# Optimization experiments

Measured on AMD Instinct MI355X. Metric: run time of the kernel, lower is better.

The kernel has to match this reference:

```python
import jax, jax.numpy as jnp
import numpy as np

N_HEAD = 16
D_MODEL = 1024
D_K = 64
D_V = 64
B = 8
L = 1024
EPS = 1e-5
NEG_INF = -1e9


def setup_inputs() -> dict:
    key = jax.random.key(0)
    ks = jax.random.split(key, 6)
    qkv_out = N_HEAD * (2 * D_K + D_V)  # 3072
    x = jax.random.normal(ks[0], (B, L, D_MODEL), dtype=jnp.float32)
    # causal attention mask (N, 1, L, L), 1 = keep, 0 = masked
    mask = jnp.broadcast_to(jnp.tril(jnp.ones((L, L), jnp.float32))[None, None], (B, 1, L, L))
    W_qkv = jax.random.normal(ks[1], (D_MODEL, qkv_out), dtype=jnp.float32) * 0.02
    b_qkv = jnp.zeros((qkv_out,), jnp.float32)
    W_proj = jax.random.normal(ks[2], (N_HEAD * D_V, D_MODEL), dtype=jnp.float32) * 0.02
    b_proj = jnp.zeros((D_MODEL,), jnp.float32)
    gamma = jnp.ones((D_MODEL,), jnp.float32)
    beta = jnp.zeros((D_MODEL,), jnp.float32)
    return {"x": x, "mask": mask, "W_qkv": W_qkv, "b_qkv": b_qkv,
            "W_proj": W_proj, "b_proj": b_proj, "gamma": gamma, "beta": beta}


def _layer_norm(x, gamma, beta):
    u = jnp.mean(x, axis=-1, keepdims=True)
    s = jnp.mean(jnp.square(x - u), axis=-1, keepdims=True)
    return gamma * (x - u) / jnp.sqrt(s + EPS) + beta


def reference(x, mask, W_qkv, b_qkv, W_proj, b_proj, gamma, beta):
    residual = x
    qkv = jnp.einsum('bld,df->blf', x, W_qkv) + b_qkv  # 1x1 Conv1D == pointwise linear
    q_l = N_HEAD * D_K
    q = qkv[:, :, :q_l]
    k = qkv[:, :, q_l:2 * q_l]
    v = qkv[:, :, 2 * q_l:]
    # split heads: (B, L, H*D) -> (B, H, L, D)
    q = q.reshape(B, L, N_HEAD, D_K).transpose(0, 2, 1, 3)
    k = k.reshape(B, L, N_HEAD, D_K).transpose(0, 2, 1, 3)
    v = v.reshape(B, L, N_HEAD, D_V).transpose(0, 2, 1, 3)
    temperature = np.power(D_K, 0.5)
    attn = jnp.einsum('bhqd,bhkd->bhqk', q, k) / temperature
    attn = mask * attn + (1.0 - mask) * NEG_INF
    attn = jax.nn.softmax(attn, axis=-1)  # dropout is identity in eval mode
    out = jnp.einsum('bhqk,bhkd->bhqd', attn, v)
    # merge heads: (B, H, L, Dv) -> (B, L, H*Dv)
    out = out.transpose(0, 2, 1, 3).reshape(B, L, N_HEAD * D_V)
    out = jnp.einsum('blf,fd->bld', out, W_proj) + b_proj
    out = _layer_norm(out + residual, gamma, beta)
    return out, attn
```

## Files before the change

### kernel.cpp

```cpp
#include <hip/hip_runtime.h>

typedef __attribute__((ext_vector_type(4))) float f32x4;
typedef __attribute__((ext_vector_type(8))) __bf16 bf16x8;
typedef __attribute__((ext_vector_type(8))) unsigned short ushort8;

static __device__ __forceinline__ unsigned short f2bf(float f) {
    unsigned int u = __float_as_uint(f);
    u += 0x7fffu + ((u >> 16) & 1u);
    return (unsigned short)(u >> 16);
}
static __device__ __forceinline__ float bf2f(unsigned short u) {
    return __uint_as_float((unsigned int)u << 16);
}
static __device__ __forceinline__ bf16x8 as_bf(ushort8 v) {
    union { ushort8 u; bf16x8 b; } x; x.u = v; return x.b;
}
static __device__ __forceinline__ void gll16(const void* g, void* l) {
    __builtin_amdgcn_global_load_lds(
        (const __attribute__((address_space(1))) void*)g,
        (__attribute__((address_space(3))) void*)l, 16, 0, 0);
}

__global__ void cvt_bf16(const float* __restrict__ in, unsigned short* __restrict__ out,
                         int n8) {
    int i = blockIdx.x * 256 + threadIdx.x;
    if (i >= n8) return;
    const float4* p = (const float4*)(in + (size_t)i * 8);
    float4 a = p[0], b = p[1];
    ushort8 o = { f2bf(a.x), f2bf(a.y), f2bf(a.z), f2bf(a.w),
                  f2bf(b.x), f2bf(b.y), f2bf(b.z), f2bf(b.w) };
    *(ushort8*)(out + (size_t)i * 8) = o;
}

__global__ void tconv_bf16(const float* __restrict__ in, unsigned short* __restrict__ out,
                           int K, int N) {
    __shared__ float t[64][65];
    const int tid = threadIdx.x;
    const int n0 = blockIdx.x * 64, k0 = blockIdx.y * 64;
#pragma unroll
    for (int i = 0; i < 4; i++) {
        int idx = tid + 256 * i;
        int r = idx >> 4, c4 = (idx & 15) * 4;
        float4 v = *(const float4*)(in + (size_t)(k0 + r) * N + n0 + c4);
        t[r][c4] = v.x; t[r][c4 + 1] = v.y; t[r][c4 + 2] = v.z; t[r][c4 + 3] = v.w;
    }
    __syncthreads();
#pragma unroll
    for (int i = 0; i < 2; i++) {
        int idx = tid + 256 * i;
        int nl = idx >> 3, k8 = (idx & 7) * 8;
        ushort8 o;
#pragma unroll
        for (int j = 0; j < 8; j++) o[j] = f2bf(t[k8 + j][nl]);
        *(ushort8*)(out + (size_t)(n0 + nl) * K + k0 + k8) = o;
    }
}

template <int EPI>
__global__ __launch_bounds__(256, 2)
void gemm_bf16(const unsigned short* __restrict__ A,
               const unsigned short* __restrict__ BT,
               const float* __restrict__ bias,
               unsigned short* __restrict__ qh, unsigned short* __restrict__ kh,
               unsigned short* __restrict__ vt,
               float* __restrict__ Cf,
               int K, int mtiles, int Ncols)
{
    __shared__ unsigned short smem[2 * 128 * 64];
    unsigned short* As = smem;
    unsigned short* Bs = smem + 128 * 64;

    const int tid = threadIdx.x;
    const int wid = tid >> 6, lane = tid & 63;
    const int g = lane >> 4, c = lane & 15;
    const int wr = (wid >> 1) * 64, wc = (wid & 1) * 64;

    const int nwg = gridDim.x;
    const int swz = ((int)blockIdx.x & 7) * (nwg >> 3) + ((int)blockIdx.x >> 3);
    const int bm = (swz % mtiles) * 128;
    const int bn = (swz / mtiles) * 128;

    const int srow = lane >> 3;
    const int scol8 = ((lane & 7) ^ srow) * 8;
    const size_t arow0 = (size_t)(bm + wid * 8 + srow);
    const size_t brow0 = (size_t)(bn + wid * 8 + srow);

    f32x4 acc[4][4] = {};

    for (int k0 = 0; k0 < K; k0 += 64) {
        __syncthreads();
#pragma unroll
        for (int t = 0; t < 4; t++) {
            gll16(A + (arow0 + t * 32) * K + k0 + scol8,
                  (char*)As + t * 4096 + wid * 1024);
            gll16(BT + (brow0 + t * 32) * K + k0 + scol8,
                  (char*)Bs + t * 4096 + wid * 1024);
        }
        __syncthreads();
#pragma unroll
        for (int ks = 0; ks < 2; ks++) {
            bf16x8 af[4], bfr[4];
#pragma unroll
            for (int mi = 0; mi < 4; mi++) {
                int row = wr + mi * 16 + c;
                int off = row * 128 + ((ks * 64 + g * 16) ^ ((c & 7) << 4));
                af[mi] = as_bf(*(const ushort8*)((const char*)As + off));
            }
#pragma unroll
            for (int ni = 0; ni < 4; ni++) {
                int row = wc + ni * 16 + c;
                int off = row * 128 + ((ks * 64 + g * 16) ^ ((c & 7) << 4));
                bfr[ni] = as_bf(*(const ushort8*)((const char*)Bs + off));
            }
#pragma unroll
            for (int mi = 0; mi < 4; mi++)
#pragma unroll
                for (int ni = 0; ni < 4; ni++)
                    acc[mi][ni] = __builtin_amdgcn_mfma_f32_16x16x32_bf16(
                        af[mi], bfr[ni], acc[mi][ni], 0, 0, 0);
        }
    }

    if (EPI == 1) {
#pragma unroll
        for (int mi = 0; mi < 4; mi++)
#pragma unroll
            for (int ni = 0; ni < 4; ni++)
#pragma unroll
                for (int r = 0; r < 4; r++) {
                    int m = bm + wr + mi * 16 + g * 4 + r;
                    int n = bn + wc + ni * 16 + c;
                    Cf[(size_t)m * Ncols + n] = acc[mi][ni][r] + bias[n];
                }
    } else {
        const int b = bm >> 10, lb = bm & 1023;
#pragma unroll
        for (int nh = 0; nh < 2; nh++) {
            int n0 = bn + nh * 64;
            int region = n0 >> 10;
            int h = (n0 & 1023) >> 6;
            __syncthreads();
            if (region < 2) {
                float qscale = (region == 0) ? 0.1803368801f : 1.0f;
                if ((wid & 1) == nh) {
#pragma unroll
                    for (int mi = 0; mi < 4; mi++)
#pragma unroll
                        for (int ni = 0; ni < 4; ni++)
#pragma unroll
                            for (int r = 0; r < 4; r++) {
                                int row = wr + mi * 16 + g * 4 + r;
                                int col = ni * 16 + c;
                                float v = (acc[mi][ni][r] + bias[n0 + col]) * qscale;
                                smem[row * 64 + col] = f2bf(v);
                            }
                }
                __syncthreads();
                unsigned short* dst = region == 0 ? qh : kh;
#pragma unroll
                for (int i = 0; i < 4; i++) {
                    int idx = tid + 256 * i;
                    int row = idx >> 3, c8 = (idx & 7) * 8;
                    ushort8 v = *(const ushort8*)&smem[row * 64 + c8];
                    *(ushort8*)(dst + ((size_t)((b * 16 + h) * 1024 + lb + row)) * 64 + c8) = v;
                }
            } else {
                if ((wid & 1) == nh) {
#pragma unroll
                    for (int mi = 0; mi < 4; mi++)
#pragma unroll
                        for (int ni = 0; ni < 4; ni++)
#pragma unroll
                            for (int r = 0; r < 4; r++) {
                                int l = wr + mi * 16 + g * 4 + r;
                                int d = ni * 16 + c;
                                float v = acc[mi][ni][r] + bias[n0 + d];
                                smem[d * 128 + (l ^ ((d & 7) << 3))] = f2bf(v);
                            }
                }
                __syncthreads();
#pragma unroll
                for (int i = 0; i < 4; i++) {
                    int idx = tid + 256 * i;
                    int d = idx >> 4, l8 = idx & 15;
                    ushort8 v = *(const ushort8*)&smem[d * 128 + ((l8 * 8) ^ ((d & 7) << 3))];
                    *(ushort8*)(vt + ((size_t)((b * 16 + h) * 64 + d)) * 1024 + lb + l8 * 8) = v;
                }
            }
        }
    }
}

__global__ __launch_bounds__(256, 2)
void attn_kernel(const unsigned short* __restrict__ qh,
                 const unsigned short* __restrict__ kh,
                 const unsigned short* __restrict__ vt,
                 float* __restrict__ attn, unsigned short* __restrict__ ob)
{
    __shared__ char smem[24576];
    char* Ks = smem;
    char* Vs = smem + 8192;
    char* Ps = smem + 16384;

    const int bh = blockIdx.x;
    const int qt = blockIdx.y;
    const int q0 = qt * 64;
    const int ntiles = qt + 1;

    const int tid = threadIdx.x, wid = tid >> 6, lane = tid & 63;
    const int g = lane >> 4, c = lane & 15;

    const size_t baseKV = (size_t)bh * 65536;
    const int qrow = q0 + wid * 16 + c;

    bf16x8 qa[2];
    qa[0] = as_bf(*(const ushort8*)(qh + baseKV + (size_t)qrow * 64 + g * 8));
    qa[1] = as_bf(*(const ushort8*)(qh + baseKV + (size_t)qrow * 64 + 32 + g * 8));

    const int srow = lane >> 3;
    const int scol8 = ((lane & 7) ^ srow) * 8;

    float lsum = 0.f;
    for (int kt = 0; kt < ntiles; ++kt) {
        const unsigned short* kb = kh + baseKV + (size_t)kt * 4096;
        __syncthreads();
        gll16(kb + (size_t)(wid * 8 + srow) * 64 + scol8, Ks + wid * 1024);
        gll16(kb + (size_t)(32 + wid * 8 + srow) * 64 + scol8, Ks + 4096 + wid * 1024);
        __syncthreads();
#pragma unroll
        for (int a = 0; a < 4; a++) {
            int krow = a * 16 + c;
            f32x4 sa = {0.f, 0.f, 0.f, 0.f};
#pragma unroll
            for (int ks = 0; ks < 2; ks++) {
                int off = krow * 128 + ((ks * 64 + g * 16) ^ ((c & 7) << 4));
                bf16x8 kf = as_bf(*(const ushort8*)(Ks + off));
                sa = __builtin_amdgcn_mfma_f32_16x16x32_bf16(kf, qa[ks], sa, 0, 0, 0);
            }
            int kb4 = kt * 64 + a * 16 + g * 4;
#pragma unroll
            for (int r = 0; r < 4; r++)
                lsum += (kb4 + r > qrow) ? 0.f : __builtin_amdgcn_exp2f(sa[r]);
        }
    }
    lsum += __shfl_xor(lsum, 16);
    lsum += __shfl_xor(lsum, 32);
    const float lr = -__log2f(lsum);

    char* Pw = Ps + wid * 2048;
    float* attnB = attn + (size_t)bh * (1024 * 1024) + (size_t)q0 * 1024;
    f32x4 oacc[4] = {};

    for (int kt = 0; kt < ntiles; ++kt) {
        const unsigned short* kb = kh + baseKV + (size_t)kt * 4096;
        const unsigned short* vb = vt + baseKV + kt * 64;
        __syncthreads();
        gll16(kb + (size_t)(wid * 8 + srow) * 64 + scol8, Ks + wid * 1024);
        gll16(kb + (size_t)(32 + wid * 8 + srow) * 64 + scol8, Ks + 4096 + wid * 1024);
        gll16(vb + (size_t)(wid * 8 + srow) * 1024 + scol8, Vs + wid * 1024);
        gll16(vb + (size_t)(32 + wid * 8 + srow) * 1024 + scol8, Vs + 4096 + wid * 1024);
        __syncthreads();

#pragma unroll
        for (int a = 0; a < 4; a++) {
            int krow = a * 16 + c;
            f32x4 sa = {0.f, 0.f, 0.f, 0.f};
#pragma unroll
            for (int ks = 0; ks < 2; ks++) {
                int off = krow * 128 + ((ks * 64 + g * 16) ^ ((c & 7) << 4));
                bf16x8 kf = as_bf(*(const ushort8*)(Ks + off));
                sa = __builtin_amdgcn_mfma_f32_16x16x32_bf16(kf, qa[ks], sa, 0, 0, 0);
            }
            int kb4 = kt * 64 + a * 16 + g * 4;
            float p0 = __builtin_amdgcn_exp2f((kb4 + 0 > qrow) ? -1e9f : sa[0] + lr);
            float p1 = __builtin_amdgcn_exp2f((kb4 + 1 > qrow) ? -1e9f : sa[1] + lr);
            float p2 = __builtin_amdgcn_exp2f((kb4 + 2 > qrow) ? -1e9f : sa[2] + lr);
            float p3 = __builtin_amdgcn_exp2f((kb4 + 3 > qrow) ? -1e9f : sa[3] + lr);
            uint2 pw;
            asm("v_cvt_pk_bf16_f32 %0, %1, %2" : "=v"(pw.x) : "v"(p0), "v"(p1));
            asm("v_cvt_pk_bf16_f32 %0, %1, %2" : "=v"(pw.y) : "v"(p2), "v"(p3));
            *(uint2*)(Pw + c * 128 + ((a * 32 + g * 8) ^ ((c & 7) << 4))) = pw;
        }

#pragma unroll
        for (int ks = 0; ks < 2; ks++) {
            int aoff = c * 128 + ((ks * 64 + g * 16) ^ ((c & 7) << 4));
            bf16x8 pa = as_bf(*(const ushort8*)(Pw + aoff));
#pragma unroll
            for (int ni = 0; ni < 4; ni++) {
                int d = ni * 16 + c;
                int voff = d * 128 + ((ks * 64 + g * 16) ^ ((d & 7) << 4));
                bf16x8 vf = as_bf(*(const ushort8*)(Vs + voff));
                oacc[ni] = __builtin_amdgcn_mfma_f32_16x16x32_bf16(pa, vf, oacc[ni], 0, 0, 0);
            }
        }
        __syncthreads();

#pragma unroll
        for (int i = 0; i < 2; i++) {
            int idx = tid + 256 * i;
            int row = idx >> 3, c16 = idx & 7;
            int off = (row >> 4) * 2048 + (row & 15) * 128 + ((c16 * 16) ^ ((row & 7) << 4));
            ushort8 v = *(const ushort8*)(Ps + off);
            float4 f0 = { bf2f(v[0]), bf2f(v[1]), bf2f(v[2]), bf2f(v[3]) };
            float4 f1 = { bf2f(v[4]), bf2f(v[5]), bf2f(v[6]), bf2f(v[7]) };
            float* dp = attnB + (size_t)row * 1024 + kt * 64 + c16 * 8;
            *(float4*)dp = f0;
            *(float4*)(dp + 4) = f1;
        }
    }

    {
        float4 z = {0.f, 0.f, 0.f, 0.f};
        for (int kt = ntiles; kt < 16; ++kt) {
#pragma unroll
            for (int i = 0; i < 4; i++) {
                int idx = tid + 256 * i;
                int row = idx >> 4, c4 = (idx & 15) << 2;
                *(float4*)(attnB + (size_t)row * 1024 + kt * 64 + c4) = z;
            }
        }
    }

    __syncthreads();
#pragma unroll
    for (int ni = 0; ni < 4; ni++)
#pragma unroll
        for (int r = 0; r < 4; r++) {
            int row = wid * 16 + g * 4 + r;
            int d = ni * 16 + c;
            int off = row * 128 + ((d * 2) ^ ((row & 7) << 4));
            *(unsigned short*)(Ks + off) = f2bf(oacc[ni][r]);
        }
    __syncthreads();
    {
        const int b = bh >> 4, h = bh & 15;
#pragma unroll
        for (int i = 0; i < 2; i++) {
            int idx = tid + 256 * i;
            int row = idx >> 3, c8 = idx & 7;
            int off = row * 128 + ((c8 * 16) ^ ((row & 7) << 4));
            ushort8 v = *(const ushort8*)(Ks + off);
            *(ushort8*)(ob + ((size_t)(b * 1024 + q0 + row)) * 1024 + h * 64 + c8 * 8) = v;
        }
    }
}

__global__ __launch_bounds__(256, 2)
void ln_kernel(const float* __restrict__ y, const float* __restrict__ x,
               const float* __restrict__ gamma, const float* __restrict__ beta,
               float* __restrict__ out)
{
    const int m = blockIdx.x;
    const int tid = threadIdx.x;
    const int wid = tid >> 6, lane = tid & 63;
    float4 vy = *(const float4*)(y + (size_t)m * 1024 + tid * 4);
    float4 vx = *(const float4*)(x + (size_t)m * 1024 + tid * 4);
    float4 v = {vy.x + vx.x, vy.y + vx.y, vy.z + vx.z, vy.w + vx.w};
    float s1 = v.x + v.y + v.z + v.w;
    float s2 = v.x * v.x + v.y * v.y + v.z * v.z + v.w * v.w;
#pragma unroll
    for (int d = 1; d < 64; d <<= 1) {
        s1 += __shfl_xor(s1, d);
        s2 += __shfl_xor(s2, d);
    }
    __shared__ float red1[4], red2[4];
    if (lane == 0) { red1[wid] = s1; red2[wid] = s2; }
    __syncthreads();
    float t1 = red1[0] + red1[1] + red1[2] + red1[3];
    float t2 = red2[0] + red2[1] + red2[2] + red2[3];
    float mean = t1 * (1.f / 1024.f);
    float var = t2 * (1.f / 1024.f) - mean * mean;
    float rstd = rsqrtf(var + 1e-5f);
    float4 g4 = *(const float4*)(gamma + tid * 4);
    float4 b4 = *(const float4*)(beta + tid * 4);
    float4 o;
    o.x = g4.x * (v.x - mean) * rstd + b4.x;
    o.y = g4.y * (v.y - mean) * rstd + b4.y;
    o.z = g4.z * (v.z - mean) * rstd + b4.z;
    o.w = g4.w * (v.w - mean) * rstd + b4.w;
    *(float4*)(out + (size_t)m * 1024 + tid * 4) = o;
}

extern "C" void kernel_launch(void* const* d_in, const int* in_sizes, int n_in,
                              void* d_out, int out_size, void* d_ws, size_t ws_size,
                              hipStream_t stream)
{
    const float* x      = (const float*)d_in[0];
    const float* W_qkv  = (const float*)d_in[2];
    const float* b_qkv  = (const float*)d_in[3];
    const float* W_proj = (const float*)d_in[4];
    const float* b_proj = (const float*)d_in[5];
    const float* gamma  = (const float*)d_in[6];
    const float* beta   = (const float*)d_in[7];

    float* out  = (float*)d_out;
    float* attn = out + (size_t)8 * 1024 * 1024;

    const size_t E = (size_t)8192 * 1024;
    unsigned short* ws = (unsigned short*)d_ws;
    unsigned short* qh     = ws;
    unsigned short* kh     = qh + E;
    unsigned short* vt     = kh + E;
    unsigned short* xb     = vt + E;
    unsigned short* wqkvT  = xb + E;
    unsigned short* wprojT = wqkvT + (size_t)3072 * 1024;
    unsigned short* ob     = wprojT + (size_t)1024 * 1024;
    float* yb   = (float*)(void*)qh;

    cvt_bf16<<<4096, 256, 0, stream>>>(x, xb, (int)(E / 8));
    tconv_bf16<<<dim3(48, 16), 256, 0, stream>>>(W_qkv, wqkvT, 1024, 3072);
    tconv_bf16<<<dim3(16, 16), 256, 0, stream>>>(W_proj, wprojT, 1024, 1024);

    gemm_bf16<0><<<1536, 256, 0, stream>>>(xb, wqkvT, b_qkv,
                                           qh, kh, vt, nullptr, 1024, 64, 3072);
    attn_kernel<<<dim3(128, 16), 256, 0, stream>>>(qh, kh, vt, attn, ob);
    gemm_bf16<1><<<512, 256, 0, stream>>>(ob, wprojT, b_proj,
                                          nullptr, nullptr, nullptr, yb, 1024, 64, 1024);
    ln_kernel<<<8192, 256, 0, stream>>>(yb, x, gamma, beta, out);
}
```

Baseline: 270.8 us.

## Double-buffer K/V/P tiles in attention kernel with prefetch and priority hints

Both attention passes now prefetch the next K (and V) tile into a second LDS buffer while the current tile is computed, so the loop needs one barrier per iteration instead of two. The P buffer is also double-buffered, which lets the attn-matrix writeback overlap the next tile's work. s_setprio raises wave priority around the MFMA sections, and launch bounds change from 2 to 3 blocks per SM. LDS use doubles to 48KB, which could limit occupancy. The correctness of the single-barrier scheme depends on the global_load_lds prefetch completing before the barrier.

```diff
diff --git a/kernel.cpp b/kernel.cpp
--- a/kernel.cpp
+++ b/kernel.cpp
@@ -191,16 +191,13 @@
     }
 }
 
-__global__ __launch_bounds__(256, 2)
+__global__ __launch_bounds__(256, 3)
 void attn_kernel(const unsigned short* __restrict__ qh,
                  const unsigned short* __restrict__ kh,
                  const unsigned short* __restrict__ vt,
                  float* __restrict__ attn, unsigned short* __restrict__ ob)
 {
-    __shared__ char smem[24576];
-    char* Ks = smem;
-    char* Vs = smem + 8192;
-    char* Ps = smem + 16384;
+    __shared__ char smem[49152];
 
     const int bh = blockIdx.x;
     const int qt = blockIdx.y;
@@ -221,92 +218,123 @@
     const int scol8 = ((lane & 7) ^ srow) * 8;
 
     float lsum = 0.f;
-    for (int kt = 0; kt < ntiles; ++kt) {
-        const unsigned short* kb = kh + baseKV + (size_t)kt * 4096;
+    {
+        int cur = 0;
+        const unsigned short* kb0 = kh + baseKV;
+        gll16(kb0 + (size_t)(wid * 8 + srow) * 64 + scol8, smem + wid * 1024);
+        gll16(kb0 + (size_t)(32 + wid * 8 + srow) * 64 + scol8, smem + 4096 + wid * 1024);
         __syncthreads();
-        gll16(kb + (size_t)(wid * 8 + srow) * 64 + scol8, Ks + wid * 1024);
-        gll16(kb + (size_t)(32 + wid * 8 + srow) * 64 + scol8, Ks + 4096 + wid * 1024);
-        __syncthreads();
-#pragma unroll
-        for (int a = 0; a < 4; a++) {
-            int krow = a * 16 + c;
-            f32x4 sa = {0.f, 0.f, 0.f, 0.f};
-#pragma unroll
-            for (int ks = 0; ks < 2; ks++) {
-                int off = krow * 128 + ((ks * 64 + g * 16) ^ ((c & 7) << 4));
-                bf16x8 kf = as_bf(*(const ushort8*)(Ks + off));
-                sa = __builtin_amdgcn_mfma_f32_16x16x32_bf16(kf, qa[ks], sa, 0, 0, 0);
-            }
-            int kb4 = kt * 64 + a * 16 + g * 4;
-#pragma unroll
-            for (int r = 0; r < 4; r++)
-                lsum += (kb4 + r > qrow) ? 0.f : __builtin_amdgcn_exp2f(sa[r]);
+        for (int kt = 0; kt < ntiles; ++kt) {
+            if (kt + 1 < ntiles) {
+                const unsigned short* kb = kh + baseKV + (size_t)(kt + 1) * 4096;
+                char* dst = smem + (cur ^ 1) * 8192;
+                gll16(kb + (size_t)(wid * 8 + srow) * 64 + scol8, dst + wid * 1024);
+                gll16(kb + (size_t)(32 + wid * 8 + srow) * 64 + scol8, dst + 4096 + wid * 1024);
+            }
+            const char* Kc = smem + cur * 8192;
+            __builtin_amdgcn_s_setprio(1);
+#pragma unroll
+            for (int a = 0; a < 4; a++) {
+                int krow = a * 16 + c;
+                f32x4 sa = {0.f, 0.f, 0.f, 0.f};
+#pragma unroll
+                for (int ks = 0; ks < 2; ks++) {
+                    int off = krow * 128 + ((ks * 64 + g * 16) ^ ((c & 7) << 4));
+                    bf16x8 kf = as_bf(*(const ushort8*)(Kc + off));
+                    sa = __builtin_amdgcn_mfma_f32_16x16x32_bf16(kf, qa[ks], sa, 0, 0, 0);
+                }
+                int kb4 = kt * 64 + a * 16 + g * 4;
+#pragma unroll
+                for (int r = 0; r < 4; r++)
+                    lsum += (kb4 + r > qrow) ? 0.f : __builtin_amdgcn_exp2f(sa[r]);
+            }
+            __builtin_amdgcn_s_setprio(0);
+            __syncthreads();
+            cur ^= 1;
         }
     }
     lsum += __shfl_xor(lsum, 16);
     lsum += __shfl_xor(lsum, 32);
     const float lr = -__log2f(lsum);
 
-    char* Pw = Ps + wid * 2048;
     float* attnB = attn + (size_t)bh * (1024 * 1024) + (size_t)q0 * 1024;
     f32x4 oacc[4] = {};
-
-    for (int kt = 0; kt < ntiles; ++kt) {
-        const unsigned short* kb = kh + baseKV + (size_t)kt * 4096;
-        const unsigned short* vb = vt + baseKV + kt * 64;
+    {
+        int cur = 0;
+        const unsigned short* kb0 = kh + baseKV;
+        const unsigned short* vb0 = vt + baseKV;
+        gll16(kb0 + (size_t)(wid * 8 + srow) * 64 + scol8, smem + wid * 1024);
+        gll16(kb0 + (size_t)(32 + wid * 8 + srow) * 64 + scol8, smem + 4096 + wid * 1024);
+        gll16(vb0 + (size_t)(wid * 8 + srow) * 1024 + scol8, smem + 16384 + wid * 1024);
+        gll16(vb0 + (size_t)(32 + wid * 8 + srow) * 1024 + scol8, smem + 20480 + wid * 1024);
         __syncthreads();
-        gll16(kb + (size_t)(wid * 8 + srow) * 64 + scol8, Ks + wid * 1024);
-        gll16(kb + (size_t)(32 + wid * 8 + srow) * 64 + scol8, Ks + 4096 + wid * 1024);
-        gll16(vb + (size_t)(wid * 8 + srow) * 1024 + scol8, Vs + wid * 1024);
-        gll16(vb + (size_t)(32 + wid * 8 + srow) * 1024 + scol8, Vs + 4096 + wid * 1024);
-        __syncthreads();
-
-#pragma unroll
-        for (int a = 0; a < 4; a++) {
-            int krow = a * 16 + c;
-            f32x4 sa = {0.f, 0.f, 0.f, 0.f};
+
+        for (int kt = 0; kt < ntiles; ++kt) {
+            if (kt + 1 < ntiles) {
+                const unsigned short* kb = kh + baseKV + (size_t)(kt + 1) * 4096;
+                const unsigned short* vb = vt + baseKV + (kt + 1) * 64;
+                char* kdst = smem + (cur ^ 1) * 8192;
+                char* vdst = smem + 16384 + (cur ^ 1) * 8192;
+                gll16(kb + (size_t)(wid * 8 + srow) * 64 + scol8, kdst + wid * 1024);
+                gll16(kb + (size_t)(32 + wid * 8 + srow) * 64 + scol8, kdst + 4096 + wid * 1024);
+                gll16(vb + (size_t)(wid * 8 + srow) * 1024 + scol8, vdst + wid * 1024);
+                gll16(vb + (size_t)(32 + wid * 8 + srow) * 1024 + scol8, vdst + 4096 + wid * 1024);
+            }
+            const char* Kc = smem + cur * 8192;
+            const char* Vc = smem + 16384 + cur * 8192;
+            char* Pc = smem + 32768 + cur * 8192;
+            char* Pw = Pc + wid * 2048;
+
+#pragma unroll
+            for (int a = 0; a < 4; a++) {
+                int krow = a * 16 + c;
+                f32x4 sa = {0.f, 0.f, 0.f, 0.f};
+#pragma unroll
+                for (int ks = 0; ks < 2; ks++) {
+                    int off = krow * 128 + ((ks * 64 + g * 16) ^ ((c & 7) << 4));
+                    bf16x8 kf = as_bf(*(const ushort8*)(Kc + off));
+                    sa = __builtin_amdgcn_mfma_f32_16x16x32_bf16(kf, qa[ks], sa, 0, 0, 0);
+                }
+                int kb4 = kt * 64 + a * 16 + g * 4;
+                float p0 = __builtin_amdgcn_exp2f((kb4 + 0 > qrow) ? -1e9f : sa[0] + lr);
+                float p1 = __builtin_amdgcn_exp2f((kb4 + 1 > qrow) ? -1e9f : sa[1] + lr);
+                float p2 = __builtin_amdgcn_exp2f((kb4 + 2 > qrow) ? -1e9f : sa[2] + lr);
+                float p3 = __builtin_amdgcn_exp2f((kb4 + 3 > qrow) ? -1e9f : sa[3] + lr);
+                uint2 pw;
+                asm("v_cvt_pk_bf16_f32 %0, %1, %2" : "=v"(pw.x) : "v"(p0), "v"(p1));
+                asm("v_cvt_pk_bf16_f32 %0, %1, %2" : "=v"(pw.y) : "v"(p2), "v"(p3));
+                *(uint2*)(Pw + c * 128 + ((a * 32 + g * 8) ^ ((c & 7) << 4))) = pw;
+            }
+
+            __builtin_amdgcn_s_setprio(1);
 #pragma unroll
             for (int ks = 0; ks < 2; ks++) {
-                int off = krow * 128 + ((ks * 64 + g * 16) ^ ((c & 7) << 4));
-                bf16x8 kf = as_bf(*(const ushort8*)(Ks + off));
-                sa = __builtin_amdgcn_mfma_f32_16x16x32_bf16(kf, qa[ks], sa, 0, 0, 0);
-            }
-            int kb4 = kt * 64 + a * 16 + g * 4;
-            float p0 = __builtin_amdgcn_exp2f((kb4 + 0 > qrow) ? -1e9f : sa[0] + lr);
-            float p1 = __builtin_amdgcn_exp2f((kb4 + 1 > qrow) ? -1e9f : sa[1] + lr);
-            float p2 = __builtin_amdgcn_exp2f((kb4 + 2 > qrow) ? -1e9f : sa[2] + lr);
-            float p3 = __builtin_amdgcn_exp2f((kb4 + 3 > qrow) ? -1e9f : sa[3] + lr);
-            uint2 pw;
-            asm("v_cvt_pk_bf16_f32 %0, %1, %2" : "=v"(pw.x) : "v"(p0), "v"(p1));
-            asm("v_cvt_pk_bf16_f32 %0, %1, %2" : "=v"(pw.y) : "v"(p2), "v"(p3));
-            *(uint2*)(Pw + c * 128 + ((a * 32 + g * 8) ^ ((c & 7) << 4))) = pw;
-        }
-
-#pragma unroll
-        for (int ks = 0; ks < 2; ks++) {
-            int aoff = c * 128 + ((ks * 64 + g * 16) ^ ((c & 7) << 4));
-            bf16x8 pa = as_bf(*(const ushort8*)(Pw + aoff));
-#pragma unroll
-            for (int ni = 0; ni < 4; ni++) {
-                int d = ni * 16 + c;
-                int voff = d * 128 + ((ks * 64 + g * 16) ^ ((d & 7) << 4));
-                bf16x8 vf = as_bf(*(const ushort8*)(Vs + voff));
-                oacc[ni] = __builtin_amdgcn_mfma_f32_16x16x32_bf16(pa, vf, oacc[ni], 0, 0, 0);
-            }
-        }
-        __syncthreads();
-
-#pragma unroll
-        for (int i = 0; i < 2; i++) {
-            int idx = tid + 256 * i;
-            int row = idx >> 3, c16 = idx & 7;
-            int off = (row >> 4) * 2048 + (row & 15) * 128 + ((c16 * 16) ^ ((row & 7) << 4));
-            ushort8 v = *(const ushort8*)(Ps + off);
-            float4 f0 = { bf2f(v[0]), bf2f(v[1]), bf2f(v[2]), bf2f(v[3]) };
-            float4 f1 = { bf2f(v[4]), bf2f(v[5]), bf2f(v[6]), bf2f(v[7]) };
-            float* dp = attnB + (size_t)row * 1024 + kt * 64 + c16 * 8;
-            *(float4*)dp = f0;
-            *(float4*)(dp + 4) = f1;
+                int aoff = c * 128 + ((ks * 64 + g * 16) ^ ((c & 7) << 4));
+                bf16x8 pa = as_bf(*(const ushort8*)(Pw + aoff));
+#pragma unroll
+                for (int ni = 0; ni < 4; ni++) {
+                    int d = ni * 16 + c;
+                    int voff = d * 128 + ((ks * 64 + g * 16) ^ ((d & 7) << 4));
+                    bf16x8 vf = as_bf(*(const ushort8*)(Vc + voff));
+                    oacc[ni] = __builtin_amdgcn_mfma_f32_16x16x32_bf16(pa, vf, oacc[ni], 0, 0, 0);
+                }
+            }
+            __builtin_amdgcn_s_setprio(0);
+            __syncthreads();
+
+#pragma unroll
+            for (int i = 0; i < 2; i++) {
+                int idx = tid + 256 * i;
+                int row = idx >> 3, c16 = idx & 7;
+                int off = (row >> 4) * 2048 + (row & 15) * 128 + ((c16 * 16) ^ ((row & 7) << 4));
+                ushort8 v = *(const ushort8*)(Pc + off);
+                float4 f0 = { bf2f(v[0]), bf2f(v[1]), bf2f(v[2]), bf2f(v[3]) };
+                float4 f1 = { bf2f(v[4]), bf2f(v[5]), bf2f(v[6]), bf2f(v[7]) };
+                float* dp = attnB + (size_t)row * 1024 + kt * 64 + c16 * 8;
+                *(float4*)dp = f0;
+                *(float4*)(dp + 4) = f1;
+            }
+            cur ^= 1;
         }
     }
 
@@ -330,7 +358,7 @@
             int row = wid * 16 + g * 4 + r;
             int d = ni * 16 + c;
             int off = row * 128 + ((d * 2) ^ ((row & 7) << 4));
-            *(unsigned short*)(Ks + off) = f2bf(oacc[ni][r]);
+            *(unsigned short*)(smem + off) = f2bf(oacc[ni][r]);
         }
     __syncthreads();
     {
@@ -340,7 +368,7 @@
             int idx = tid + 256 * i;
             int row = idx >> 3, c8 = idx & 7;
             int off = row * 128 + ((c8 * 16) ^ ((row & 7) << 4));
-            ushort8 v = *(const ushort8*)(Ks + off);
+            ushort8 v = *(const ushort8*)(smem + off);
             *(ushort8*)(ob + ((size_t)(b * 1024 + q0 + row)) * 1024 + h * 64 + c8 * 8) = v;
         }
     }
```

New measurement: 273.1 us. Within noise of the previous version (+0.9%).
